# Kernel optimization log

Measured on AMD Instinct MI355X. Metric: run time of the kernel, lower is better.

Reference implementation:

```python
import jax, jax.numpy as jnp
import numpy as np

B, C, H, W = 2, 64, 512, 512
HEADS = 4
EPS = 1e-12  # F.normalize eps


def setup_inputs() -> dict:
    key = jax.random.key(0)
    ks = jax.random.split(key, 7)
    s = 0.02
    return {
        "x": jax.random.normal(ks[0], (B, C, H, W), jnp.float32),
        "Wq": jax.random.normal(ks[1], (C, C), jnp.float32) * s,
        "Wk": jax.random.normal(ks[2], (C, C), jnp.float32) * s,
        "Wv": jax.random.normal(ks[3], (C, C), jnp.float32) * s,
        "Wp": jax.random.normal(ks[4], (C, C), jnp.float32) * s,
        "bp": jax.random.normal(ks[5], (C,), jnp.float32) * s,
        "rescale": jnp.ones((HEADS, 1, 1), jnp.float32),
    }


def reference(x, Wq, Wk, Wv, Wp, bp, rescale):
    b, c, h, w = x.shape
    n = h * w
    d = c // HEADS
    xf = x.reshape(b, c, n)  # 1x1 conv == channel matmul on flattened spatial

    def conv1x1(Wt):
        return jnp.einsum('oc,bcn->bon', Wt, xf)

    # torch: permute->reshape(b,n,c)->split heads->transpose == reshape conv out to (b,heads,d,n)
    q = conv1x1(Wq).reshape(b, HEADS, d, n)
    k = conv1x1(Wk).reshape(b, HEADS, d, n)
    v = conv1x1(Wv).reshape(b, HEADS, d, n)

    def l2norm(t):  # F.normalize(p=2, dim=-1)
        nrm = jnp.sqrt(jnp.sum(t * t, axis=-1, keepdims=True))
        return t / jnp.maximum(nrm, EPS)

    q = l2norm(q)
    k = l2norm(k)

    attn = jnp.einsum('bhdn,bhen->bhde', k, q)  # (b, heads, d, d) tiny matrix
    attn = attn * rescale  # rescale broadcasts (heads,1,1)
    attn = jax.nn.softmax(attn, axis=-1)

    o = jnp.einsum('bhde,bhen->bhdn', attn, v).reshape(b, c, n)
    out = jnp.einsum('oc,bcn->bon', Wp, o) + bp[None, :, None] + xf  # proj + residual
    return out.reshape(b, c, h, w)
```

## Files before the change

kernel.cpp:

```cpp
#include <hip/hip_runtime.h>
#include <math.h>

#define C 64
#define NHEADS 4
#define DH 16
#define NN 262144
#define NB 2
#define PB 512
#define NT 2
#define EPS 1e-12f

typedef __attribute__((ext_vector_type(8))) short short8v;
typedef __attribute__((ext_vector_type(8))) unsigned short ushort8v;
typedef __attribute__((ext_vector_type(4))) unsigned short ushort4v;
typedef __attribute__((ext_vector_type(4))) float f32x4;

static __device__ __forceinline__ unsigned short f2bf(float f) {
  union { float f; unsigned int u; } v; v.f = f;
  unsigned int r = v.u + 0x7fffu + ((v.u >> 16) & 1u);
  return (unsigned short)(r >> 16);
}

__global__ __launch_bounds__(256, 2) void gram_kernel(const float* __restrict__ x,
                                                      float* __restrict__ Gc) {
  __shared__ unsigned short xs[C * 256];
  const int b = blockIdx.y;
  const int chunk = blockIdx.x;
  const float* xb = x + (size_t)b * C * NN;
  const int t = threadIdx.x;
  const int w = t >> 6, l = t & 63;
  const int lrow = l & 15, lhi = l >> 4;

  const int gA0 = (w >> 1) * 2, gA1 = gA0 + 1;
  const int gB0 = (w & 1) * 2,  gB1 = gB0 + 1;
  const int cA0 = gA0 * 16 + lrow, cA1 = gA1 * 16 + lrow;
  const int cB0 = gB0 * 16 + lrow, cB1 = gB1 * 16 + lrow;

  f32x4 acc0 = {0.f,0.f,0.f,0.f}, acc1 = {0.f,0.f,0.f,0.f};
  f32x4 acc2 = {0.f,0.f,0.f,0.f}, acc3 = {0.f,0.f,0.f,0.f};

  for (int tile = 0; tile < NT; ++tile) {
    const int j0 = (chunk * NT + tile) * 256;
    __syncthreads();
#pragma unroll
    for (int i = 0; i < 8; ++i) {
      const int oi = i * 256 + t;
      const int c = oi >> 5, oct = oi & 31;
      const float* src = xb + (size_t)c * NN + j0 + oct * 8;
      const float4 v0 = *reinterpret_cast<const float4*>(src);
      const float4 v1 = *reinterpret_cast<const float4*>(src + 4);
      ushort8v pk;
      pk[0] = f2bf(v0.x); pk[1] = f2bf(v0.y); pk[2] = f2bf(v0.z); pk[3] = f2bf(v0.w);
      pk[4] = f2bf(v1.x); pk[5] = f2bf(v1.y); pk[6] = f2bf(v1.z); pk[7] = f2bf(v1.w);
      *reinterpret_cast<ushort8v*>(&xs[c * 256 + ((oct ^ (c & 7)) << 3)]) = pk;
    }
    __syncthreads();
#pragma unroll
    for (int s = 0; s < 8; ++s) {
      const int o = s * 4 + lhi;
      const short8v fA0 = *reinterpret_cast<const short8v*>(&xs[cA0 * 256 + ((o ^ (cA0 & 7)) << 3)]);
      const short8v fA1 = *reinterpret_cast<const short8v*>(&xs[cA1 * 256 + ((o ^ (cA1 & 7)) << 3)]);
      const short8v fB0 = *reinterpret_cast<const short8v*>(&xs[cB0 * 256 + ((o ^ (cB0 & 7)) << 3)]);
      const short8v fB1 = *reinterpret_cast<const short8v*>(&xs[cB1 * 256 + ((o ^ (cB1 & 7)) << 3)]);
      acc0 = __builtin_amdgcn_mfma_f32_16x16x32_bf16(fA0, fB0, acc0, 0, 0, 0);
      acc1 = __builtin_amdgcn_mfma_f32_16x16x32_bf16(fA0, fB1, acc1, 0, 0, 0);
      acc2 = __builtin_amdgcn_mfma_f32_16x16x32_bf16(fA1, fB0, acc2, 0, 0, 0);
      acc3 = __builtin_amdgcn_mfma_f32_16x16x32_bf16(fA1, fB1, acc3, 0, 0, 0);
    }
  }
  float* g = Gc + ((size_t)b * PB + chunk) * 4096;
#pragma unroll
  for (int r = 0; r < 4; ++r) {
    const int row = lhi * 4 + r;
    g[(gA0 * 16 + row) * 64 + gB0 * 16 + lrow] = acc0[r];
    g[(gA0 * 16 + row) * 64 + gB1 * 16 + lrow] = acc1[r];
    g[(gA1 * 16 + row) * 64 + gB0 * 16 + lrow] = acc2[r];
    g[(gA1 * 16 + row) * 64 + gB1 * 16 + lrow] = acc3[r];
  }
}

__global__ __launch_bounds__(256) void reduce_kernel(const float* __restrict__ Gc,
                                                     float* __restrict__ G) {
  __shared__ float s[4][64];
  const int b = blockIdx.y;
  const int g = blockIdx.x;
  const int t = threadIdx.x;
  const int e = g * 64 + (t & 63);
  const int chunk = t >> 6;
  float sum = 0.f;
  for (int p = chunk; p < PB; p += 4)
    sum += Gc[((size_t)b * PB + p) * 4096 + e];
  s[chunk][t & 63] = sum;
  __syncthreads();
  if (t < 64) G[(size_t)b * 4096 + g * 64 + t] = s[0][t] + s[1][t] + s[2][t] + s[3][t];
}

__global__ __launch_bounds__(256) void attn_kernel(const float* __restrict__ G,
    const float* __restrict__ Wq, const float* __restrict__ Wk,
    const float* __restrict__ Wv, const float* __restrict__ Wp,
    const float* __restrict__ rescale, unsigned short* __restrict__ Ebf) {
  __shared__ float Gs[4096], GQt[4096], GKt[4096], T[4096];
  __shared__ float attnw[64][DH];
  __shared__ float nq[64], nk[64];
  const int b = blockIdx.x;
  const int t = threadIdx.x;

  for (int i = t; i < 4096; i += 256) Gs[i] = G[(size_t)b * 4096 + i];
  __syncthreads();
  for (int i = t; i < 4096; i += 256) {
    const int c = i >> 6, e = i & 63;
    float sq_ = 0.f, sk_ = 0.f;
    for (int c2 = 0; c2 < 64; ++c2) {
      const float g = Gs[c * 64 + c2];
      sq_ += g * Wq[e * 64 + c2];
      sk_ += g * Wk[e * 64 + c2];
    }
    GQt[c * 64 + e] = sq_;
    GKt[c * 64 + e] = sk_;
  }
  __syncthreads();
  if (t < 64) {
    float s = 0.f;
    for (int c2 = 0; c2 < 64; ++c2) s += Wq[t * 64 + c2] * GQt[c2 * 64 + t];
    nq[t] = sqrtf(fmaxf(s, 0.f));
  } else if (t < 128) {
    const int d = t - 64;
    float s = 0.f;
    for (int c2 = 0; c2 < 64; ++c2) s += Wk[d * 64 + c2] * GKt[c2 * 64 + d];
    nk[d] = sqrtf(fmaxf(s, 0.f));
  }
  __syncthreads();
  if (t < 64) {
    const int h = t >> 4;
    const float rs = rescale[h];
    const float nkd = fmaxf(nk[t], EPS);
    float logits[DH];
    float mx = -1e30f;
    for (int ee = 0; ee < DH; ++ee) {
      const int e = h * DH + ee;
      float num = 0.f;
      for (int c2 = 0; c2 < 64; ++c2) num += Wk[t * 64 + c2] * GQt[c2 * 64 + e];
      const float l = num / (nkd * fmaxf(nq[e], EPS)) * rs;
      logits[ee] = l;
      mx = fmaxf(mx, l);
    }
    float sum = 0.f;
    for (int ee = 0; ee < DH; ++ee) { const float p = expf(logits[ee] - mx); logits[ee] = p; sum += p; }
    const float inv = 1.f / sum;
    for (int ee = 0; ee < DH; ++ee) attnw[t][ee] = logits[ee] * inv;
  }
  __syncthreads();
  for (int i = t; i < 4096; i += 256) {
    const int r = i >> 6, c = i & 63;
    const int h = r >> 4;
    float s = 0.f;
    for (int e = 0; e < DH; ++e) s += attnw[r][e] * Wv[(h * DH + e) * 64 + c];
    T[i] = s;
  }
  __syncthreads();
  for (int i = t; i < 4096; i += 256) {
    const int r = i >> 6, c = i & 63;
    float s = (r == c) ? 1.f : 0.f;
    for (int m = 0; m < 64; ++m) s += Wp[r * 64 + m] * T[m * 64 + c];
    Ebf[(size_t)b * 4096 + i] = f2bf(s);
  }
}

__global__ __launch_bounds__(256, 4) void apply_kernel(const float* __restrict__ x,
    const unsigned short* __restrict__ Ebf, const float* __restrict__ bp,
    float* __restrict__ out) {
  __shared__ unsigned short xt[128 * 64];
  const int b = blockIdx.y;
  const int n0 = blockIdx.x * 128;
  const float* xb = x + (size_t)b * C * NN;
  float* ob = out + (size_t)b * C * NN;
  const int t = threadIdx.x;
  const int w = t >> 6, l = t & 63;
  const int lrow = l & 15, lhi = l >> 4;

  short8v ef[4][2];
  const unsigned short* eb = Ebf + (size_t)b * 4096;
#pragma unroll
  for (int ot = 0; ot < 4; ++ot)
#pragma unroll
    for (int ks = 0; ks < 2; ++ks)
      ef[ot][ks] = *reinterpret_cast<const short8v*>(eb + (ot * 16 + lrow) * 64 + ks * 32 + lhi * 8);

#pragma unroll
  for (int h = 0; h < 2; ++h) {
    const int n = h * 64 + l;
#pragma unroll
    for (int i = 0; i < 4; ++i) {
      const int c0 = w * 16 + i * 4;
      const float v0 = xb[(size_t)(c0 + 0) * NN + n0 + n];
      const float v1 = xb[(size_t)(c0 + 1) * NN + n0 + n];
      const float v2 = xb[(size_t)(c0 + 2) * NN + n0 + n];
      const float v3 = xb[(size_t)(c0 + 3) * NN + n0 + n];
      ushort4v pk;
      pk[0] = f2bf(v0); pk[1] = f2bf(v1); pk[2] = f2bf(v2); pk[3] = f2bf(v3);
      const int q = c0 >> 2;
      *reinterpret_cast<ushort4v*>(
          &xt[n * 64 + ((((q >> 1) ^ (n & 7)) << 3) + (q & 1) * 4)]) = pk;
    }
  }
  __syncthreads();

  f32x4 acc[4][2];
#pragma unroll
  for (int ot = 0; ot < 4; ++ot)
#pragma unroll
    for (int nn = 0; nn < 2; ++nn) acc[ot][nn] = (f32x4){0.f, 0.f, 0.f, 0.f};

  const int nbase = w * 32;
#pragma unroll
  for (int nn = 0; nn < 2; ++nn) {
    const int n = nbase + nn * 16 + lrow;
#pragma unroll
    for (int ks = 0; ks < 2; ++ks) {
      const int s = ks * 4 + lhi;
      const short8v xf = *reinterpret_cast<const short8v*>(&xt[n * 64 + ((s ^ (n & 7)) << 3)]);
#pragma unroll
      for (int ot = 0; ot < 4; ++ot)
        acc[ot][nn] = __builtin_amdgcn_mfma_f32_16x16x32_bf16(ef[ot][ks], xf, acc[ot][nn], 0, 0, 0);
    }
  }

#pragma unroll
  for (int ot = 0; ot < 4; ++ot) {
#pragma unroll
    for (int r = 0; r < 4; ++r) {
      const int o = ot * 16 + lhi * 4 + r;
      const float bias = bp[o];
#pragma unroll
      for (int nn = 0; nn < 2; ++nn) {
        const int n = nbase + nn * 16 + lrow;
        ob[(size_t)o * NN + n0 + n] = acc[ot][nn][r] + bias;
      }
    }
  }
}

extern "C" void kernel_launch(void* const* d_in, const int* in_sizes, int n_in,
                              void* d_out, int out_size, void* d_ws, size_t ws_size,
                              hipStream_t stream) {
  const float* x       = (const float*)d_in[0];
  const float* Wq      = (const float*)d_in[1];
  const float* Wk      = (const float*)d_in[2];
  const float* Wv      = (const float*)d_in[3];
  const float* Wp      = (const float*)d_in[4];
  const float* bp      = (const float*)d_in[5];
  const float* rescale = (const float*)d_in[6];
  float* out = (float*)d_out;

  float* Gc = out;
  float* G  = (float*)d_ws;
  unsigned short* Ebf = (unsigned short*)(G + (size_t)NB * 4096);

  gram_kernel<<<dim3(PB, NB), dim3(256), 0, stream>>>(x, Gc);
  reduce_kernel<<<dim3(64, NB), dim3(256), 0, stream>>>(Gc, G);
  attn_kernel<<<dim3(NB), dim3(256), 0, stream>>>(G, Wq, Wk, Wv, Wp, rescale, Ebf);
  apply_kernel<<<dim3(2048, NB), dim3(256), 0, stream>>>(x, Ebf, bp, out);
}
```

Baseline: 155.7 us.

## Prefetch gram tiles into registers and vectorize apply-kernel output stores

The gram kernel now loads the next tile's fp32 data into registers while the current tile sits in LDS for MFMA work, replacing __syncthreads with explicit waitcnt and barrier, and asks for 3 blocks per SM instead of 2. The apply kernel swaps the MFMA operands so each lane holds four consecutive spatial outputs, which allows float4 stores instead of scalar ones. Per-chunk Gram partials move from the output buffer into the workspace. The extra prefetch registers may limit the requested occupancy.

```diff
diff --git a/kernel.cpp b/kernel.cpp
--- a/kernel.cpp
+++ b/kernel.cpp
@@ -21,7 +21,7 @@
   return (unsigned short)(r >> 16);
 }
 
-__global__ __launch_bounds__(256, 2) void gram_kernel(const float* __restrict__ x,
+__global__ __launch_bounds__(256, 3) void gram_kernel(const float* __restrict__ x,
                                                       float* __restrict__ Gc) {
   __shared__ unsigned short xs[C * 256];
   const int b = blockIdx.y;
@@ -30,6 +30,7 @@
   const int t = threadIdx.x;
   const int w = t >> 6, l = t & 63;
   const int lrow = l & 15, lhi = l >> 4;
+  const int sc = t >> 5, soct = t & 31;
 
   const int gA0 = (w >> 1) * 2, gA1 = gA0 + 1;
   const int gB0 = (w & 1) * 2,  gB1 = gB0 + 1;
@@ -39,22 +40,38 @@
   f32x4 acc0 = {0.f,0.f,0.f,0.f}, acc1 = {0.f,0.f,0.f,0.f};
   f32x4 acc2 = {0.f,0.f,0.f,0.f}, acc3 = {0.f,0.f,0.f,0.f};
 
+  float4 pre[8][2];
+#pragma unroll
+  for (int i = 0; i < 8; ++i) {
+    const int c = i * 8 + sc;
+    const float* src = xb + (size_t)c * NN + chunk * (NT * 256) + soct * 8;
+    pre[i][0] = *reinterpret_cast<const float4*>(src);
+    pre[i][1] = *reinterpret_cast<const float4*>(src + 4);
+  }
+
   for (int tile = 0; tile < NT; ++tile) {
-    const int j0 = (chunk * NT + tile) * 256;
-    __syncthreads();
 #pragma unroll
     for (int i = 0; i < 8; ++i) {
-      const int oi = i * 256 + t;
-      const int c = oi >> 5, oct = oi & 31;
-      const float* src = xb + (size_t)c * NN + j0 + oct * 8;
-      const float4 v0 = *reinterpret_cast<const float4*>(src);
-      const float4 v1 = *reinterpret_cast<const float4*>(src + 4);
+      const int c = i * 8 + sc;
       ushort8v pk;
-      pk[0] = f2bf(v0.x); pk[1] = f2bf(v0.y); pk[2] = f2bf(v0.z); pk[3] = f2bf(v0.w);
-      pk[4] = f2bf(v1.x); pk[5] = f2bf(v1.y); pk[6] = f2bf(v1.z); pk[7] = f2bf(v1.w);
-      *reinterpret_cast<ushort8v*>(&xs[c * 256 + ((oct ^ (c & 7)) << 3)]) = pk;
-    }
-    __syncthreads();
+      pk[0] = f2bf(pre[i][0].x); pk[1] = f2bf(pre[i][0].y);
+      pk[2] = f2bf(pre[i][0].z); pk[3] = f2bf(pre[i][0].w);
+      pk[4] = f2bf(pre[i][1].x); pk[5] = f2bf(pre[i][1].y);
+      pk[6] = f2bf(pre[i][1].z); pk[7] = f2bf(pre[i][1].w);
+      *reinterpret_cast<ushort8v*>(&xs[c * 256 + ((soct ^ (c & 7)) << 3)]) = pk;
+    }
+    if (tile + 1 < NT) {
+      const int j0 = chunk * (NT * 256) + (tile + 1) * 256;
+#pragma unroll
+      for (int i = 0; i < 8; ++i) {
+        const int c = i * 8 + sc;
+        const float* src = xb + (size_t)c * NN + j0 + soct * 8;
+        pre[i][0] = *reinterpret_cast<const float4*>(src);
+        pre[i][1] = *reinterpret_cast<const float4*>(src + 4);
+      }
+    }
+    asm volatile("s_waitcnt lgkmcnt(0)" ::: "memory");
+    __builtin_amdgcn_s_barrier();
 #pragma unroll
     for (int s = 0; s < 8; ++s) {
       const int o = s * 4 + lhi;
@@ -67,6 +84,8 @@
       acc2 = __builtin_amdgcn_mfma_f32_16x16x32_bf16(fA1, fB0, acc2, 0, 0, 0);
       acc3 = __builtin_amdgcn_mfma_f32_16x16x32_bf16(fA1, fB1, acc3, 0, 0, 0);
     }
+    asm volatile("s_waitcnt lgkmcnt(0)" ::: "memory");
+    __builtin_amdgcn_s_barrier();
   }
   float* g = Gc + ((size_t)b * PB + chunk) * 4096;
 #pragma unroll
@@ -221,21 +240,23 @@
       const short8v xf = *reinterpret_cast<const short8v*>(&xt[n * 64 + ((s ^ (n & 7)) << 3)]);
 #pragma unroll
       for (int ot = 0; ot < 4; ++ot)
-        acc[ot][nn] = __builtin_amdgcn_mfma_f32_16x16x32_bf16(ef[ot][ks], xf, acc[ot][nn], 0, 0, 0);
+        acc[ot][nn] = __builtin_amdgcn_mfma_f32_16x16x32_bf16(xf, ef[ot][ks], acc[ot][nn], 0, 0, 0);
     }
   }
 
 #pragma unroll
   for (int ot = 0; ot < 4; ++ot) {
-#pragma unroll
-    for (int r = 0; r < 4; ++r) {
-      const int o = ot * 16 + lhi * 4 + r;
-      const float bias = bp[o];
-#pragma unroll
-      for (int nn = 0; nn < 2; ++nn) {
-        const int n = nbase + nn * 16 + lrow;
-        ob[(size_t)o * NN + n0 + n] = acc[ot][nn][r] + bias;
-      }
+    const int o = ot * 16 + lrow;
+    const float bias = bp[o];
+#pragma unroll
+    for (int nn = 0; nn < 2; ++nn) {
+      const int nb4 = nbase + nn * 16 + lhi * 4;
+      float4 o4;
+      o4.x = acc[ot][nn][0] + bias;
+      o4.y = acc[ot][nn][1] + bias;
+      o4.z = acc[ot][nn][2] + bias;
+      o4.w = acc[ot][nn][3] + bias;
+      *reinterpret_cast<float4*>(&ob[(size_t)o * NN + n0 + nb4]) = o4;
     }
   }
 }
@@ -252,8 +273,8 @@
   const float* rescale = (const float*)d_in[6];
   float* out = (float*)d_out;
 
-  float* Gc = out;
-  float* G  = (float*)d_ws;
+  float* Gc = (float*)d_ws;
+  float* G  = Gc + (size_t)NB * PB * 4096;
   unsigned short* Ebf = (unsigned short*)(G + (size_t)NB * 4096);
 
   gram_kernel<<<dim3(PB, NB), dim3(256), 0, stream>>>(x, Gc);
```

Result: slower. 161.3 us (+3.6%).
